# Kernel optimization log

Hardware: AMD Instinct MI355X
Metric: run time of the kernel (lower is better)

## Reference

```python
import jax, jax.numpy as jnp
import numpy as np

IN_F = 4096
OUT_F = 4096
Q_LEVELS = 16  # 4-bit


def setup_inputs() -> dict:
    key = jax.random.key(0)
    k = jax.random.split(key, 7)
    input = jax.random.normal(k[0], (4, 128, IN_F), dtype=jnp.float32)
    qweight = jax.random.randint(k[1], (OUT_F, IN_F), 0, Q_LEVELS, dtype=jnp.int32)
    scales = jax.random.uniform(k[2], (OUT_F, 1), dtype=jnp.float32)
    zeros = jax.random.uniform(k[3], (OUT_F, 1), dtype=jnp.float32)
    outlier = jax.random.uniform(k[4], (OUT_F, IN_F), dtype=jnp.float32)
    grad_updates = jax.random.normal(k[5], (OUT_F, IN_F), dtype=jnp.float32)
    bias = jax.random.normal(k[6], (OUT_F,), dtype=jnp.float32)
    return {"input": input, "qweight": qweight, "scales": scales,
            "zeros": zeros, "outlier": outlier,
            "grad_updates": grad_updates, "bias": bias}


def reference(input, qweight, scales, zeros, outlier, grad_updates, bias):
    # dequantize: affine per-output-row quantization -> dense weight [out, in]
    weight = (qweight.astype(jnp.float32) - zeros) * scales
    # sparse outlier correction (densified), scaled by learned GradUpdates
    weight = weight + outlier * grad_updates
    # F.linear: y = x @ W^T + b
    return jnp.einsum('bsi,oi->bso', input, weight) + bias
```

## Files before the change

### kernel.cpp

```cpp
#include <hip/hip_runtime.h>
#include <stdint.h>

#define IN_F   4096
#define OUT_F  4096
#define M_TOT  512
#define KT     (IN_F / 32)
#define BN     16
#define BK     128
#define KSPLIT 2
#define KPB    (IN_F / KSPLIT)
#define NITER  (KPB / BK)

typedef unsigned short u16;
typedef __bf16 bf16x8 __attribute__((ext_vector_type(8)));
typedef float  f32x4  __attribute__((ext_vector_type(4)));

__device__ __forceinline__ u16 f2bf(float x) {
    unsigned u = __float_as_uint(x);
    u += 0x7FFFu + ((u >> 16) & 1u);
    return (u16)(u >> 16);
}

__global__ void pack_a_kernel(const float* __restrict__ in, u16* __restrict__ aws) {
    int t    = blockIdx.x * blockDim.x + threadIdx.x;
    int lane = t & 63;
    int kt   = (t >> 6) & (KT - 1);
    int mt   = t >> 13;
    int m = mt * 16 + (lane & 15);
    int k = kt * 32 + ((lane >> 4) << 3);
    const float* src = in + (size_t)m * IN_F + k;
    float4 a0 = *(const float4*)src;
    float4 a1 = *(const float4*)(src + 4);
    union { u16 u[8]; uint4 v; } pk;
    pk.u[0]=f2bf(a0.x); pk.u[1]=f2bf(a0.y); pk.u[2]=f2bf(a0.z); pk.u[3]=f2bf(a0.w);
    pk.u[4]=f2bf(a1.x); pk.u[5]=f2bf(a1.y); pk.u[6]=f2bf(a1.z); pk.u[7]=f2bf(a1.w);
    *(uint4*)(aws + (size_t)t * 8) = pk.v;
}

__global__ __launch_bounds__(512, 4) void qlinear_kernel(
    const u16*   __restrict__ aws,
    const int*   __restrict__ qw,
    const float* __restrict__ scales,
    const float* __restrict__ zeros,
    const float* __restrict__ outlier,
    const float* __restrict__ grad,
    float*       __restrict__ part)
{
    __shared__ __align__(16) u16 Bsh[2][4 * 64 * 8];

    const int tid  = threadIdx.x;
    const int lane = tid & 63;
    const int wv   = tid >> 6;

    const int nblk  = blockIdx.x >> 1;
    const int khalf = blockIdx.x & 1;
    const int n0    = nblk * BN;
    const int k0    = khalf * KPB;

    const int srow = tid >> 5;
    const int schk = tid & 31;
    const int orow = n0 + srow;
    const float sr = scales[orow];
    const float c0 = -zeros[orow] * sr;
    const size_t sg = (size_t)orow * IN_F + k0 + schk * 4;
    const int sks   = schk >> 3;
    const int squad = (schk >> 1) & 3;
    const int j0    = (schk & 1) * 4;
    const int slane = srow | (squad << 4);
    const int doff  = (sks * 64 + slane) * 8 + j0;

    int4 qb[2]; float4 ob[2], gb[2];
    auto ld = [&](int it) {
        int s = it & 1;
        size_t off = sg + (size_t)it * BK;
        qb[s] = *(const int4*)  (qw      + off);
        ob[s] = *(const float4*)(outlier + off);
        gb[s] = *(const float4*)(grad    + off);
    };
    auto st = [&](int it) {
        int s = it & 1;
        union { u16 u[4]; uint2 v; } pk;
        pk.u[0] = f2bf(fmaf((float)qb[s].x, sr, fmaf(ob[s].x, gb[s].x, c0)));
        pk.u[1] = f2bf(fmaf((float)qb[s].y, sr, fmaf(ob[s].y, gb[s].y, c0)));
        pk.u[2] = f2bf(fmaf((float)qb[s].z, sr, fmaf(ob[s].z, gb[s].z, c0)));
        pk.u[3] = f2bf(fmaf((float)qb[s].w, sr, fmaf(ob[s].w, gb[s].w, c0)));
        *(uint2*)(&Bsh[it & 1][doff]) = pk.v;
    };

    const u16* abase = aws + ((size_t)(wv * 4) * KT + khalf * (KPB / 32)) * 512
                           + (size_t)lane * 8;

    f32x4 acc[4] = {};

    ld(0);
    st(0);
    ld(1);
    __syncthreads();

    for (int it = 0; it < NITER; ++it) {
        const u16* bb = &Bsh[it & 1][0];
        bf16x8 bfr[4];
        #pragma unroll
        for (int ks = 0; ks < 4; ++ks)
            bfr[ks] = *(const bf16x8*)(bb + (ks * 64 + lane) * 8);

        #pragma unroll
        for (int ks = 0; ks < 4; ++ks) {
            #pragma unroll
            for (int mf = 0; mf < 4; ++mf) {
                bf16x8 af = *(const bf16x8*)(abase + ((size_t)mf * KT + it * 4 + ks) * 512);
                acc[mf] = __builtin_amdgcn_mfma_f32_16x16x32_bf16(af, bfr[ks], acc[mf], 0, 0, 0);
            }
        }

        if (it + 1 < NITER) st(it + 1);
        if (it + 2 < NITER) ld(it + 2);
        __syncthreads();
    }

    float* pout = part + (size_t)khalf * (M_TOT * OUT_F);
    const int cm0 = wv * 64 + ((lane >> 4) << 2);
    const int cn  = n0 + (lane & 15);
    #pragma unroll
    for (int mf = 0; mf < 4; ++mf) {
        #pragma unroll
        for (int r = 0; r < 4; ++r)
            pout[(size_t)(cm0 + mf * 16 + r) * OUT_F + cn] = acc[mf][r];
    }
}

__global__ void reduce_kernel(const float4* __restrict__ part,
                              const float4* __restrict__ bias,
                              float4* __restrict__ out) {
    int idx = blockIdx.x * blockDim.x + threadIdx.x;
    float4 s = bias[idx & (OUT_F / 4 - 1)];
    const int STRIDE = M_TOT * OUT_F / 4;
    #pragma unroll
    for (int k = 0; k < KSPLIT; ++k) {
        float4 p = part[(size_t)k * STRIDE + idx];
        s.x += p.x; s.y += p.y; s.z += p.z; s.w += p.w;
    }
    out[idx] = s;
}

extern "C" void kernel_launch(void* const* d_in, const int* in_sizes, int n_in,
                              void* d_out, int out_size, void* d_ws, size_t ws_size,
                              hipStream_t stream) {
    const float* input   = (const float*)d_in[0];
    const int*   qweight = (const int*)  d_in[1];
    const float* scales  = (const float*)d_in[2];
    const float* zeros   = (const float*)d_in[3];
    const float* outlier = (const float*)d_in[4];
    const float* grad    = (const float*)d_in[5];
    const float* bias    = (const float*)d_in[6];
    float* out = (float*)d_out;

    u16*   aws  = (u16*)d_ws;
    float* part = (float*)((char*)d_ws + (4u << 20));

    pack_a_kernel<<<(M_TOT * IN_F / 8) / 256, 256, 0, stream>>>(input, aws);
    qlinear_kernel<<<(OUT_F / BN) * KSPLIT, 512, 0, stream>>>(
        aws, qweight, scales, zeros, outlier, grad, part);
    reduce_kernel<<<(M_TOT * OUT_F / 4) / 256, 256, 0, stream>>>(
        (const float4*)part, (const float4*)bias, (float4*)out);
}
```

Measured before the change: 235.1 us.

## Widen N tile to 64, split K four ways, use nontemporal streaming loads

Each block now covers 64 output columns with 1024 threads (16 waves of 32 rows each) and a 64-wide K step, and K is split into four parts instead of two. Each A fragment loaded from global memory now feeds four MFMAs instead of one, so the bf16 activation stream is re-read less often. Weight, outlier and grad streams use nontemporal loads, and partial outputs use nontemporal stores, to keep them out of cache. The cost is twice the partial-sum buffer traffic in the reduce kernel and larger blocks, which may limit occupancy.

```diff
diff --git a/kernel.cpp b/kernel.cpp
--- a/kernel.cpp
+++ b/kernel.cpp
@@ -5,15 +5,17 @@
 #define OUT_F  4096
 #define M_TOT  512
 #define KT     (IN_F / 32)
-#define BN     16
-#define BK     128
-#define KSPLIT 2
+#define BN     64
+#define BK     64
+#define KSPLIT 4
 #define KPB    (IN_F / KSPLIT)
 #define NITER  (KPB / BK)
 
 typedef unsigned short u16;
 typedef __bf16 bf16x8 __attribute__((ext_vector_type(8)));
 typedef float  f32x4  __attribute__((ext_vector_type(4)));
+typedef int    i32x4  __attribute__((ext_vector_type(4)));
+typedef float  fv4    __attribute__((ext_vector_type(4)));
 
 __device__ __forceinline__ u16 f2bf(float x) {
     unsigned u = __float_as_uint(x);
@@ -37,7 +39,7 @@
     *(uint4*)(aws + (size_t)t * 8) = pk.v;
 }
 
-__global__ __launch_bounds__(512, 4) void qlinear_kernel(
+__global__ __launch_bounds__(1024, 4) void qlinear_kernel(
     const u16*   __restrict__ aws,
     const int*   __restrict__ qw,
     const float* __restrict__ scales,
@@ -46,19 +48,19 @@
     const float* __restrict__ grad,
     float*       __restrict__ part)
 {
-    __shared__ __align__(16) u16 Bsh[2][4 * 64 * 8];
+    __shared__ __align__(16) u16 Bsh[2][8 * 64 * 8];
 
     const int tid  = threadIdx.x;
     const int lane = tid & 63;
     const int wv   = tid >> 6;
 
-    const int nblk  = blockIdx.x >> 1;
-    const int khalf = blockIdx.x & 1;
-    const int n0    = nblk * BN;
-    const int k0    = khalf * KPB;
+    const int nblk = blockIdx.x >> 2;
+    const int kq   = blockIdx.x & 3;
+    const int n0   = nblk * BN;
+    const int k0   = kq * KPB;
 
-    const int srow = tid >> 5;
-    const int schk = tid & 31;
+    const int srow = tid >> 4;
+    const int schk = tid & 15;
     const int orow = n0 + srow;
     const float sr = scales[orow];
     const float c0 = -zeros[orow] * sr;
@@ -66,16 +68,17 @@
     const int sks   = schk >> 3;
     const int squad = (schk >> 1) & 3;
     const int j0    = (schk & 1) * 4;
-    const int slane = srow | (squad << 4);
-    const int doff  = (sks * 64 + slane) * 8 + j0;
+    const int snf   = srow >> 4;
+    const int slane = (srow & 15) | (squad << 4);
+    const int doff  = ((sks * 4 + snf) * 64 + slane) * 8 + j0;
 
-    int4 qb[2]; float4 ob[2], gb[2];
+    i32x4 qb[2]; fv4 ob[2], gb[2];
     auto ld = [&](int it) {
         int s = it & 1;
         size_t off = sg + (size_t)it * BK;
-        qb[s] = *(const int4*)  (qw      + off);
-        ob[s] = *(const float4*)(outlier + off);
-        gb[s] = *(const float4*)(grad    + off);
+        qb[s] = __builtin_nontemporal_load((const i32x4*)(qw      + off));
+        ob[s] = __builtin_nontemporal_load((const fv4*)  (outlier + off));
+        gb[s] = __builtin_nontemporal_load((const fv4*)  (grad    + off));
     };
     auto st = [&](int it) {
         int s = it & 1;
@@ -87,10 +90,10 @@
         *(uint2*)(&Bsh[it & 1][doff]) = pk.v;
     };
 
-    const u16* abase = aws + ((size_t)(wv * 4) * KT + khalf * (KPB / 32)) * 512
+    const u16* abase = aws + ((size_t)(wv * 2) * KT + kq * (KPB / 32)) * 512
                            + (size_t)lane * 8;
 
-    f32x4 acc[4] = {};
+    f32x4 acc[2][4] = {};
 
     ld(0);
     st(0);
@@ -98,19 +101,26 @@
     __syncthreads();
 
     for (int it = 0; it < NITER; ++it) {
+        bf16x8 af[2][2];
+        #pragma unroll
+        for (int ks = 0; ks < 2; ++ks)
+            #pragma unroll
+            for (int mf = 0; mf < 2; ++mf)
+                af[ks][mf] = *(const bf16x8*)(abase + ((size_t)mf * KT + it * 2 + ks) * 512);
+
         const u16* bb = &Bsh[it & 1][0];
-        bf16x8 bfr[4];
         #pragma unroll
-        for (int ks = 0; ks < 4; ++ks)
-            bfr[ks] = *(const bf16x8*)(bb + (ks * 64 + lane) * 8);
-
-        #pragma unroll
-        for (int ks = 0; ks < 4; ++ks) {
+        for (int ks = 0; ks < 2; ++ks) {
+            bf16x8 bfr[4];
             #pragma unroll
-            for (int mf = 0; mf < 4; ++mf) {
-                bf16x8 af = *(const bf16x8*)(abase + ((size_t)mf * KT + it * 4 + ks) * 512);
-                acc[mf] = __builtin_amdgcn_mfma_f32_16x16x32_bf16(af, bfr[ks], acc[mf], 0, 0, 0);
-            }
+            for (int nf = 0; nf < 4; ++nf)
+                bfr[nf] = *(const bf16x8*)(bb + (((ks * 4 + nf) * 64) + lane) * 8);
+            #pragma unroll
+            for (int mf = 0; mf < 2; ++mf)
+                #pragma unroll
+                for (int nf = 0; nf < 4; ++nf)
+                    acc[mf][nf] = __builtin_amdgcn_mfma_f32_16x16x32_bf16(
+                        af[ks][mf], bfr[nf], acc[mf][nf], 0, 0, 0);
         }
 
         if (it + 1 < NITER) st(it + 1);
@@ -118,27 +128,30 @@
         __syncthreads();
     }
 
-    float* pout = part + (size_t)khalf * (M_TOT * OUT_F);
-    const int cm0 = wv * 64 + ((lane >> 4) << 2);
+    float* pout = part + (size_t)kq * (M_TOT * OUT_F);
+    const int cm0 = wv * 32 + ((lane >> 4) << 2);
     const int cn  = n0 + (lane & 15);
     #pragma unroll
-    for (int mf = 0; mf < 4; ++mf) {
+    for (int mf = 0; mf < 2; ++mf)
         #pragma unroll
-        for (int r = 0; r < 4; ++r)
-            pout[(size_t)(cm0 + mf * 16 + r) * OUT_F + cn] = acc[mf][r];
-    }
+        for (int nf = 0; nf < 4; ++nf)
+            #pragma unroll
+            for (int r = 0; r < 4; ++r)
+                __builtin_nontemporal_store(
+                    acc[mf][nf][r],
+                    pout + (size_t)(cm0 + mf * 16 + r) * OUT_F + cn + nf * 16);
 }
 
-__global__ void reduce_kernel(const float4* __restrict__ part,
-                              const float4* __restrict__ bias,
-                              float4* __restrict__ out) {
+__global__ void reduce_kernel(const fv4* __restrict__ part,
+                              const fv4* __restrict__ bias,
+                              fv4* __restrict__ out) {
     int idx = blockIdx.x * blockDim.x + threadIdx.x;
-    float4 s = bias[idx & (OUT_F / 4 - 1)];
+    fv4 s = bias[idx & (OUT_F / 4 - 1)];
     const int STRIDE = M_TOT * OUT_F / 4;
     #pragma unroll
     for (int k = 0; k < KSPLIT; ++k) {
-        float4 p = part[(size_t)k * STRIDE + idx];
-        s.x += p.x; s.y += p.y; s.z += p.z; s.w += p.w;
+        fv4 p = __builtin_nontemporal_load(part + (size_t)k * STRIDE + idx);
+        s += p;
     }
     out[idx] = s;
 }
@@ -159,8 +172,8 @@
     float* part = (float*)((char*)d_ws + (4u << 20));
 
     pack_a_kernel<<<(M_TOT * IN_F / 8) / 256, 256, 0, stream>>>(input, aws);
-    qlinear_kernel<<<(OUT_F / BN) * KSPLIT, 512, 0, stream>>>(
+    qlinear_kernel<<<(OUT_F / BN) * KSPLIT, 1024, 0, stream>>>(
         aws, qweight, scales, zeros, outlier, grad, part);
     reduce_kernel<<<(M_TOT * OUT_F / 4) / 256, 256, 0, stream>>>(
-        (const float4*)part, (const float4*)bias, (float4*)out);
+        (const fv4*)part, (const fv4*)bias, (fv4*)out);
 }
```

Measured after the change: 220.0 us. 1.07x faster.
